# Performance work log

Hardware: AMD Instinct MI355X
Metric: run time of the kernel (lower is better)

## Reference

```python
import jax, jax.numpy as jnp
import numpy as np

N = 100000          # nodes
E = 300000          # edges
F_IN = 128          # num_features
H = 256             # hidden_size
C = 1               # num_classes
G = 2048            # number of graphs in batch
EPS = 1e-5


def setup_inputs() -> dict:
    key = jax.random.key(0)
    ks = jax.random.split(key, 16)
    x = jax.random.normal(ks[0], (N, F_IN), dtype=jnp.float32)
    edge_index = jax.random.randint(ks[1], (2, E), 0, N, dtype=jnp.int64)
    batch = jnp.sort(jax.random.randint(ks[2], (N,), 0, G, dtype=jnp.int64))

    def glorot(k, shape):
        lim = np.sqrt(6.0 / (shape[0] + shape[1]))
        return jax.random.uniform(k, shape, jnp.float32, -lim, lim)

    return {
        "x": x, "edge_index": edge_index, "batch": batch,
        "W1": glorot(ks[3], (F_IN, H)), "b1": jnp.zeros((H,), jnp.float32),
        "W2": glorot(ks[4], (H, H)),    "b2": jnp.zeros((H,), jnp.float32),
        "W3": glorot(ks[5], (H, H)),    "b3": jnp.zeros((H,), jnp.float32),
        "g1": jnp.ones((H,), jnp.float32),  "be1": jnp.zeros((H,), jnp.float32),
        "g2": jnp.ones((H,), jnp.float32),  "be2": jnp.zeros((H,), jnp.float32),
        "g3": jnp.ones((H,), jnp.float32),  "be3": jnp.zeros((H,), jnp.float32),
        "LW1": glorot(ks[6], (H, H)),   "Lb1": jnp.zeros((H,), jnp.float32),
        "LW2": glorot(ks[7], (H, C)),   "Lb2": jnp.zeros((C,), jnp.float32),
    }


def _gcn_conv(x, W, b, src, dst, dinv):
    xw = x @ W                                       # [N, H]
    coeff = (dinv[src] * dinv[dst])[:, None]          # [E, 1]
    msg = xw[src] * coeff                             # gather + scale, [E, H]
    agg = jax.ops.segment_sum(msg, dst, num_segments=x.shape[0])  # scatter-add
    agg = agg + xw * (dinv * dinv)[:, None]           # self-loop term
    return agg + b


def _bn_relu(h, g, be):
    # BatchNorm1d in training mode: batch stats over nodes (biased variance)
    m = h.mean(axis=0)
    v = h.var(axis=0)
    return jax.nn.relu((h - m) * jax.lax.rsqrt(v + EPS) * g + be)


def reference(x, edge_index, batch, W1, b1, W2, b2, W3, b3,
              g1, be1, g2, be2, g3, be3, LW1, Lb1, LW2, Lb2):
    src = edge_index[0]
    dst = edge_index[1]
    # degree with self-loops (computed at destination, as in PyG)
    deg = jax.ops.segment_sum(jnp.ones((E,), jnp.float32), dst, num_segments=N) + 1.0
    dinv = jax.lax.rsqrt(deg)

    h = _bn_relu(_gcn_conv(x, W1, b1, src, dst, dinv), g1, be1)
    h = _bn_relu(_gcn_conv(h, W2, b2, src, dst, dinv), g2, be2)
    h = _bn_relu(_gcn_conv(h, W3, b3, src, dst, dinv), g3, be3)

    # global_add_pool: sum node features per graph
    pooled = jax.ops.segment_sum(h, batch, num_segments=G)   # [G, H]

    out = jax.nn.relu(pooled @ LW1 + Lb1)
    out = out @ LW2 + Lb2                                    # [G, 1]
    return jnp.squeeze(out, axis=1)                          # [G]
```

## Files before the change

### kernel.cpp

```cpp
#include <hip/hip_runtime.h>


typedef __attribute__((ext_vector_type(8))) short bf16x8;
typedef __attribute__((ext_vector_type(4))) float f32x4;

__device__ inline float bf2f(unsigned short u) {
    union { unsigned int i; float f; } v; v.i = ((unsigned int)u) << 16; return v.f;
}
__device__ inline unsigned short f2bf(float f) {
    unsigned int x = __float_as_uint(f);
    unsigned int r = (x + 0x7FFFu + ((x >> 16) & 1u)) >> 16;
    return (unsigned short)r;
}

__device__ inline float4 ld4u(const unsigned short* p) {
    ushort4 u = *(const ushort4*)(p);
    return make_float4(bf2f(u.x), bf2f(u.y), bf2f(u.z), bf2f(u.w));
}
__device__ inline void st4u(unsigned short* p, float4 v) {
    ushort4 u; u.x = f2bf(v.x); u.y = f2bf(v.y); u.z = f2bf(v.z); u.w = f2bf(v.w);
    *(ushort4*)p = u;
}

__global__ void count_deg_i(const int* __restrict__ dst, int* __restrict__ deg, int E) {
    int i = blockIdx.x * blockDim.x + threadIdx.x;
    int stride = gridDim.x * blockDim.x;
    for (; i < E; i += stride) atomicAdd(&deg[dst[i]], 1);
}

__global__ __launch_bounds__(256) void scan_partial(
    const int* __restrict__ deg, int* __restrict__ psum, int N)
{
    __shared__ int red[256];
    const int t = threadIdx.x;
    const int i0 = blockIdx.x * 512 + t * 2;
    int s = 0;
    if (i0 < N) s += deg[i0];
    if (i0 + 1 < N) s += deg[i0 + 1];
    red[t] = s;
    __syncthreads();
    for (int off = 128; off > 0; off >>= 1) {
        if (t < off) red[t] += red[t + off];
        __syncthreads();
    }
    if (t == 0) psum[blockIdx.x] = red[0];
}

__global__ __launch_bounds__(1024) void scan_offsets(
    const int* __restrict__ psum, int* __restrict__ poff, int NB,
    int* __restrict__ rowptr, int N)
{
    __shared__ int s[1024];
    const int t = threadIdx.x;
    int v = (t < NB) ? psum[t] : 0;
    s[t] = v;
    __syncthreads();
    for (int off = 1; off < 1024; off <<= 1) {
        int u = (t >= off) ? s[t - off] : 0;
        __syncthreads();
        s[t] += u;
        __syncthreads();
    }
    if (t < NB) poff[t] = s[t] - v;
    if (t == 1023) rowptr[N] = s[1023];
}

__global__ __launch_bounds__(256) void write_rowptr(
    const int* __restrict__ deg, const int* __restrict__ poff,
    int* __restrict__ rowptr, int N)
{
    __shared__ int s[256];
    const int t = threadIdx.x;
    const int i0 = blockIdx.x * 512 + t * 2;
    int e0 = (i0 < N) ? deg[i0] : 0;
    int e1 = (i0 + 1 < N) ? deg[i0 + 1] : 0;
    int sum = e0 + e1;
    s[t] = sum;
    __syncthreads();
    for (int off = 1; off < 256; off <<= 1) {
        int u = (t >= off) ? s[t - off] : 0;
        __syncthreads();
        s[t] += u;
        __syncthreads();
    }
    int excl = s[t] - sum + poff[blockIdx.x];
    if (i0 < N) rowptr[i0] = excl;
    if (i0 + 1 < N) rowptr[i0 + 1] = excl + e0;
}

__global__ void dinv_from_rowptr(const int* __restrict__ rowptr, float* __restrict__ dinv, int N) {
    int i = blockIdx.x * blockDim.x + threadIdx.x;
    if (i < N) dinv[i] = rsqrtf((float)(rowptr[i + 1] - rowptr[i]) + 1.0f);
}

__global__ void fill_csr(const int* __restrict__ src, const int* __restrict__ dst,
                         const int* __restrict__ rowptr, int* __restrict__ cnt,
                         int* __restrict__ col, int E)
{
    int i = blockIdx.x * blockDim.x + threadIdx.x;
    int stride = gridDim.x * blockDim.x;
    for (; i < E; i += stride) {
        int d = dst[i];
        int pos = atomicAdd(&cnt[d], 1);
        col[rowptr[d] + pos] = src[i];
    }
}

__global__ void conv_bf16(const float* __restrict__ in, unsigned short* __restrict__ out,
                          size_t n4)
{
    size_t i = blockIdx.x * (size_t)blockDim.x + threadIdx.x;
    size_t stride = (size_t)gridDim.x * blockDim.x;
    const float4* in4 = (const float4*)in;
    for (; i < n4; i += stride) {
        float4 v = in4[i];
        st4u(out + i * 4, v);
    }
}

__global__ void make_wt(const float* __restrict__ W, unsigned short* __restrict__ WT, int K) {
    int i = blockIdx.x * blockDim.x + threadIdx.x;
    if (i < K * 256) {
        int k = i >> 8, n = i & 255;
        WT[n * K + k] = f2bf(W[i]);
    }
}

__device__ inline unsigned int bn2(unsigned int w, float sL, float hL, float sH, float hH) {
    float lo = bf2f((unsigned short)(w & 0xFFFFu));
    float hi = bf2f((unsigned short)(w >> 16));
    lo = fmaxf(fmaf(lo, sL, hL), 0.f);
    hi = fmaxf(fmaf(hi, sH, hH), 0.f);
    return (unsigned int)f2bf(lo) | ((unsigned int)f2bf(hi) << 16);
}
__device__ inline uint4 bn8(uint4 v, const float* __restrict__ ss, int c) {
    float4 sA = *(const float4*)(ss + c);
    float4 sB = *(const float4*)(ss + c + 4);
    float4 hA = *(const float4*)(ss + 256 + c);
    float4 hB = *(const float4*)(ss + 256 + c + 4);
    uint4 r;
    r.x = bn2(v.x, sA.x, hA.x, sA.y, hA.y);
    r.y = bn2(v.y, sA.z, hA.z, sA.w, hA.w);
    r.z = bn2(v.z, sB.x, hB.x, sB.y, hB.y);
    r.w = bn2(v.w, sB.z, hB.z, sB.w, hB.w);
    return r;
}

template<int FUSE_BN>
__global__ __launch_bounds__(256) void gemm_mfma(
    const unsigned short* __restrict__ A,
    const unsigned short* __restrict__ WT,
    const float* __restrict__ dinv,
    const float* __restrict__ ss,
    unsigned short* __restrict__ C,
    int K)
{
    __shared__ unsigned short As[128 * 32];
    __shared__ unsigned short Bs[128 * 32];

    const int tid = threadIdx.x;
    const int bm = blockIdx.x * 128;
    const int bn = blockIdx.y * 128;
    const int lane = tid & 63;
    const int wid = tid >> 6;
    const int wr = wid >> 1;
    const int wc = wid & 1;

    const int r0 = tid >> 2;
    const int cc0 = tid & 3;

    f32x4 acc[4][4];
    #pragma unroll
    for (int m = 0; m < 4; ++m)
        #pragma unroll
        for (int n = 0; n < 4; ++n)
            acc[m][n] = (f32x4){0.f, 0.f, 0.f, 0.f};

    uint4* AsV = (uint4*)As;
    uint4* BsV = (uint4*)Bs;

    for (int k0 = 0; k0 < K; k0 += 32) {
        if (k0) __syncthreads();
        {
            const int gcc = (cc0 ^ (r0 & 3)) * 8;
            uint4 va0 = *(const uint4*)(A  + (size_t)(bm + r0)      * K + k0 + gcc);
            uint4 vb0 = *(const uint4*)(WT + (size_t)(bn + r0)      * K + k0 + gcc);
            uint4 va1 = *(const uint4*)(A  + (size_t)(bm + r0 + 64) * K + k0 + gcc);
            uint4 vb1 = *(const uint4*)(WT + (size_t)(bn + r0 + 64) * K + k0 + gcc);
            if (FUSE_BN) {
                va0 = bn8(va0, ss, k0 + gcc);
                va1 = bn8(va1, ss, k0 + gcc);
            }
            AsV[r0 * 4 + cc0]        = va0;
            AsV[(r0 + 64) * 4 + cc0] = va1;
            BsV[r0 * 4 + cc0]        = vb0;
            BsV[(r0 + 64) * 4 + cc0] = vb1;
        }
        __syncthreads();

        bf16x8 af[4], bfv[4];
        #pragma unroll
        for (int n = 0; n < 4; ++n) {
            int R = wc * 64 + n * 16 + (lane & 15);
            int pc = (lane >> 4) ^ (R & 3);
            af[n] = *(const bf16x8*)&Bs[R * 32 + pc * 8];
        }
        #pragma unroll
        for (int m = 0; m < 4; ++m) {
            int R = wr * 64 + m * 16 + (lane & 15);
            int pc = (lane >> 4) ^ (R & 3);
            bfv[m] = *(const bf16x8*)&As[R * 32 + pc * 8];
        }
        #pragma unroll
        for (int m = 0; m < 4; ++m)
            #pragma unroll
            for (int n = 0; n < 4; ++n)
                acc[m][n] = __builtin_amdgcn_mfma_f32_16x16x32_bf16(
                    af[n], bfv[m], acc[m][n], 0, 0, 0);
    }

    #pragma unroll
    for (int m = 0; m < 4; ++m) {
        int row = bm + wr * 64 + m * 16 + (lane & 15);
        float di = dinv[row];
        #pragma unroll
        for (int n = 0; n < 4; ++n) {
            int cb = bn + wc * 64 + n * 16 + ((lane >> 4) << 2);
            ushort4 u;
            u.x = f2bf(acc[m][n][0] * di);
            u.y = f2bf(acc[m][n][1] * di);
            u.z = f2bf(acc[m][n][2] * di);
            u.w = f2bf(acc[m][n][3] * di);
            *(ushort4*)(C + (size_t)row * 256 + cb) = u;
        }
    }
}

__global__ __launch_bounds__(256) void gather_bn(
    const unsigned short* __restrict__ xs, const int* __restrict__ rowptr,
    const int* __restrict__ col, const float* __restrict__ dinv,
    const float* __restrict__ b, unsigned short* __restrict__ t_out,
    float* __restrict__ stats, int N)
{
    __shared__ float lred[4][512];
    const int lane = threadIdx.x & 63;
    const int wid = threadIdx.x >> 6;
    const int c4 = lane * 4;
    const float4 bv = *(const float4*)(b + c4);

    float s0 = 0, s1 = 0, s2 = 0, s3 = 0;
    float q0 = 0, q1 = 0, q2 = 0, q3 = 0;

    const int w = (blockIdx.x * blockDim.x + threadIdx.x) >> 6;
    const int nw = (gridDim.x * blockDim.x) >> 6;

    for (int n0 = w; n0 < N; n0 += nw * 4) {
        const int nA = n0;
        const int nB = n0 + nw;
        const int nC = n0 + 2 * nw;
        const int nD = n0 + 3 * nw;
        const bool hB = nB < N, hC = nC < N, hD = nD < N;

        int eA = rowptr[nA], eA1 = rowptr[nA + 1];
        int eB = 0, eB1 = 0, eC = 0, eC1 = 0, eD = 0, eD1 = 0;
        if (hB) { eB = rowptr[nB]; eB1 = rowptr[nB + 1]; }
        if (hC) { eC = rowptr[nC]; eC1 = rowptr[nC + 1]; }
        if (hD) { eD = rowptr[nD]; eD1 = rowptr[nD + 1]; }

        float4 aA = ld4u(xs + (size_t)nA * 256 + c4);
        float4 aB = make_float4(0.f, 0.f, 0.f, 0.f), aC = aB, aD = aB;
        if (hB) aB = ld4u(xs + (size_t)nB * 256 + c4);
        if (hC) aC = ld4u(xs + (size_t)nC * 256 + c4);
        if (hD) aD = ld4u(xs + (size_t)nD * 256 + c4);

        while ((eA < eA1) | (eB < eB1) | (eC < eC1) | (eD < eD1)) {
            int sA = -1, sB = -1, sC = -1, sD = -1;
            if (eA < eA1) sA = col[eA++];
            if (eB < eB1) sB = col[eB++];
            if (eC < eC1) sC = col[eC++];
            if (eD < eD1) sD = col[eD++];
            float4 vA, vB, vC, vD;
            if (sA >= 0) vA = ld4u(xs + (size_t)sA * 256 + c4);
            if (sB >= 0) vB = ld4u(xs + (size_t)sB * 256 + c4);
            if (sC >= 0) vC = ld4u(xs + (size_t)sC * 256 + c4);
            if (sD >= 0) vD = ld4u(xs + (size_t)sD * 256 + c4);
            if (sA >= 0) { aA.x += vA.x; aA.y += vA.y; aA.z += vA.z; aA.w += vA.w; }
            if (sB >= 0) { aB.x += vB.x; aB.y += vB.y; aB.z += vB.z; aB.w += vB.w; }
            if (sC >= 0) { aC.x += vC.x; aC.y += vC.y; aC.z += vC.z; aC.w += vC.w; }
            if (sD >= 0) { aD.x += vD.x; aD.y += vD.y; aD.z += vD.z; aD.w += vD.w; }
        }

        {
            float di = dinv[nA];
            float4 t;
            t.x = fmaf(di, aA.x, bv.x); t.y = fmaf(di, aA.y, bv.y);
            t.z = fmaf(di, aA.z, bv.z); t.w = fmaf(di, aA.w, bv.w);
            st4u(t_out + (size_t)nA * 256 + c4, t);
            s0 += t.x; s1 += t.y; s2 += t.z; s3 += t.w;
            q0 += t.x * t.x; q1 += t.y * t.y; q2 += t.z * t.z; q3 += t.w * t.w;
        }
        if (hB) {
            float di = dinv[nB];
            float4 t;
            t.x = fmaf(di, aB.x, bv.x); t.y = fmaf(di, aB.y, bv.y);
            t.z = fmaf(di, aB.z, bv.z); t.w = fmaf(di, aB.w, bv.w);
            st4u(t_out + (size_t)nB * 256 + c4, t);
            s0 += t.x; s1 += t.y; s2 += t.z; s3 += t.w;
            q0 += t.x * t.x; q1 += t.y * t.y; q2 += t.z * t.z; q3 += t.w * t.w;
        }
        if (hC) {
            float di = dinv[nC];
            float4 t;
            t.x = fmaf(di, aC.x, bv.x); t.y = fmaf(di, aC.y, bv.y);
            t.z = fmaf(di, aC.z, bv.z); t.w = fmaf(di, aC.w, bv.w);
            st4u(t_out + (size_t)nC * 256 + c4, t);
            s0 += t.x; s1 += t.y; s2 += t.z; s3 += t.w;
            q0 += t.x * t.x; q1 += t.y * t.y; q2 += t.z * t.z; q3 += t.w * t.w;
        }
        if (hD) {
            float di = dinv[nD];
            float4 t;
            t.x = fmaf(di, aD.x, bv.x); t.y = fmaf(di, aD.y, bv.y);
            t.z = fmaf(di, aD.z, bv.z); t.w = fmaf(di, aD.w, bv.w);
            st4u(t_out + (size_t)nD * 256 + c4, t);
            s0 += t.x; s1 += t.y; s2 += t.z; s3 += t.w;
            q0 += t.x * t.x; q1 += t.y * t.y; q2 += t.z * t.z; q3 += t.w * t.w;
        }
    }

    lred[wid][c4 + 0] = s0; lred[wid][c4 + 1] = s1;
    lred[wid][c4 + 2] = s2; lred[wid][c4 + 3] = s3;
    lred[wid][256 + c4 + 0] = q0; lred[wid][256 + c4 + 1] = q1;
    lred[wid][256 + c4 + 2] = q2; lred[wid][256 + c4 + 3] = q3;
    __syncthreads();
    for (int i = threadIdx.x; i < 512; i += 256) {
        float v = lred[0][i] + lred[1][i] + lred[2][i] + lred[3][i];
        atomicAdd(&stats[i], v);
    }
}

__global__ void bn_finalize(const float* __restrict__ stats,
                            const float* __restrict__ g, const float* __restrict__ be,
                            float* __restrict__ ss, int N)
{
    int f = threadIdx.x;
    float m = stats[f] / (float)N;
    float v = stats[256 + f] / (float)N - m * m;
    float sc = g[f] * rsqrtf(v + 1e-5f);
    ss[f] = sc;
    ss[256 + f] = be[f] - m * sc;
}

__global__ __launch_bounds__(256) void pool_seg(
    const unsigned short* __restrict__ t, const int* __restrict__ batch,
    const float* __restrict__ ss, float* __restrict__ pooled, int N)
{
    __shared__ float lred[4][256];
    const int g = blockIdx.x;
    const int lane = threadIdx.x & 63;
    const int wid = threadIdx.x >> 6;
    const int c4 = lane * 4;

    int lo = 0, hi = N;
    while (lo < hi) { int m = (lo + hi) >> 1; if (batch[m] < g) lo = m + 1; else hi = m; }
    const int start = lo;
    hi = N;
    while (lo < hi) { int m = (lo + hi) >> 1; if (batch[m] < g + 1) lo = m + 1; else hi = m; }
    const int end = lo;

    const float4 sc = *(const float4*)(ss + c4);
    const float4 sh = *(const float4*)(ss + 256 + c4);
    float4 acc = make_float4(0.f, 0.f, 0.f, 0.f);
    for (int r = start + wid; r < end; r += 4) {
        float4 a = ld4u(t + (size_t)r * 256 + c4);
        acc.x += fmaxf(fmaf(a.x, sc.x, sh.x), 0.f);
        acc.y += fmaxf(fmaf(a.y, sc.y, sh.y), 0.f);
        acc.z += fmaxf(fmaf(a.z, sc.z, sh.z), 0.f);
        acc.w += fmaxf(fmaf(a.w, sc.w, sh.w), 0.f);
    }
    lred[wid][c4 + 0] = acc.x; lred[wid][c4 + 1] = acc.y;
    lred[wid][c4 + 2] = acc.z; lred[wid][c4 + 3] = acc.w;
    __syncthreads();
    int i = threadIdx.x;
    pooled[(size_t)g * 256 + i] = lred[0][i] + lred[1][i] + lred[2][i] + lred[3][i];
}

__global__ __launch_bounds__(256) void mlp_fused(
    const float* __restrict__ pooled,
    const float* __restrict__ LW1, const float* __restrict__ Lb1,
    const float* __restrict__ LW2, const float* __restrict__ Lb2,
    float* __restrict__ out)
{
    __shared__ float sp[256];
    __shared__ float red[256];
    const int g = blockIdx.x;
    const int t = threadIdx.x;
    sp[t] = pooled[(size_t)g * 256 + t];
    __syncthreads();
    float acc = Lb1[t];
    #pragma unroll 8
    for (int k = 0; k < 256; ++k) acc = fmaf(sp[k], LW1[k * 256 + t], acc);
    acc = fmaxf(acc, 0.f);
    red[t] = acc * LW2[t];
    __syncthreads();
    for (int s = 128; s > 0; s >>= 1) {
        if (t < s) red[t] += red[t + s];
        __syncthreads();
    }
    if (t == 0) out[g] = red[0] + Lb2[0];
}

extern "C" void kernel_launch(void* const* d_in, const int* in_sizes, int n_in,
                              void* d_out, int out_size, void* d_ws, size_t ws_size,
                              hipStream_t stream)
{
    const float* x    = (const float*)d_in[0];
    const int*   ei   = (const int*)d_in[1];
    const int*   batch= (const int*)d_in[2];
    const float* W1 = (const float*)d_in[3];  const float* b1 = (const float*)d_in[4];
    const float* W2 = (const float*)d_in[5];  const float* b2 = (const float*)d_in[6];
    const float* W3 = (const float*)d_in[7];  const float* b3 = (const float*)d_in[8];
    const float* g1 = (const float*)d_in[9];  const float* be1= (const float*)d_in[10];
    const float* g2 = (const float*)d_in[11]; const float* be2= (const float*)d_in[12];
    const float* g3 = (const float*)d_in[13]; const float* be3= (const float*)d_in[14];
    const float* LW1= (const float*)d_in[15]; const float* Lb1= (const float*)d_in[16];
    const float* LW2= (const float*)d_in[17]; const float* Lb2= (const float*)d_in[18];

    const int N = in_sizes[2];
    const int E = in_sizes[1] / 2;
    const int F = in_sizes[0] / N;
    const int H = in_sizes[4];
    const int G = out_size;
    const int Mp = (N + 127) & ~127;
    const int NB = (N + 511) / 512;
    const int* src = ei;
    const int* dst = ei + E;
    const size_t NHp = (size_t)Mp * H;

    const float* Wl[3] = {W1, W2, W3};
    const float* bl[3] = {b1, b2, b3};
    const float* gl[3] = {g1, g2, g3};
    const float* bel[3]= {be1, be2, be3};

    char* p = (char*)d_ws;
    unsigned short* TB = (unsigned short*)p;  p += NHp * 2;
    unsigned short* XS = (unsigned short*)p;  p += NHp * 2;
    unsigned short* XB = (unsigned short*)p;  p += (size_t)Mp * 128 * 2;
    float* dinv = (float*)p;           p += (((size_t)Mp * 4) + 255) & ~(size_t)255;
    int* degi  = (int*)p;              p += (((size_t)N * 4) + 255) & ~(size_t)255;
    float* stats = (float*)p;          p += 2048;
    float* ss    = (float*)p;          p += 2048;
    int* psum   = (int*)p;             p += 4096;
    int* poff   = (int*)p;             p += 4096;
    float* pooled= (float*)p;          p += (size_t)G * H * 4;
    int* rowptr = (int*)p;             p += (((size_t)(N + 1) * 4) + 255) & ~(size_t)255;
    int* col    = (int*)p;             p += (((size_t)E * 4) + 255) & ~(size_t)255;
    unsigned short* WTb = (unsigned short*)p;  p += (size_t)H * H * 2;

    hipMemsetAsync(degi, 0, (size_t)N * sizeof(int), stream);
    count_deg_i<<<1024, 256, 0, stream>>>(dst, degi, E);
    scan_partial<<<NB, 256, 0, stream>>>(degi, psum, N);
    scan_offsets<<<1, 1024, 0, stream>>>(psum, poff, NB, rowptr, N);
    write_rowptr<<<NB, 256, 0, stream>>>(degi, poff, rowptr, N);
    dinv_from_rowptr<<<(N + 255) / 256, 256, 0, stream>>>(rowptr, dinv, N);
    hipMemsetAsync(degi, 0, (size_t)N * sizeof(int), stream);
    fill_csr<<<1024, 256, 0, stream>>>(src, dst, rowptr, degi, col, E);

    conv_bf16<<<2048, 256, 0, stream>>>(x, XB, (size_t)N * F / 4);

    for (int L = 0; L < 3; ++L) {
        const int K = (L == 0) ? F : H;
        make_wt<<<(K * 256 + 255) / 256, 256, 0, stream>>>(Wl[L], WTb, K);
        dim3 grid(Mp / 128, H / 128);
        if (L == 0)
            gemm_mfma<0><<<grid, 256, 0, stream>>>(XB, WTb, dinv, nullptr, XS, K);
        else
            gemm_mfma<1><<<grid, 256, 0, stream>>>(TB, WTb, dinv, ss, XS, K);
        hipMemsetAsync(stats, 0, 512 * sizeof(float), stream);
        gather_bn<<<1024, 256, 0, stream>>>(XS, rowptr, col, dinv, bl[L], TB, stats, N);
        bn_finalize<<<1, 256, 0, stream>>>(stats, gl[L], bel[L], ss, N);
    }

    pool_seg<<<G, 256, 0, stream>>>(TB, batch, ss, pooled, N);
    mlp_fused<<<G, 256, 0, stream>>>(pooled, LW1, Lb1, LW2, Lb2, (float*)d_out);
}
```

Baseline: 594.0 us.

## Aggregate before transform in layer one, fuse pool+MLP, batch weight prep

Layer one now aggregates the 128-wide input features over the graph before the GEMM (A·X·W ordering), so the sparse gather moves 128 columns instead of 256. Because of that it needs a separate stats pass over the GEMM output. All three weight transposes are combined into one launch. Pooling and the MLP head are fused into one kernel handling 8 graphs per block. Stats zeroing moves into bn_finalize, the GEMM gets a grouped block-index remap, and the gather grid size doubles. This changes rounding order and adds an extra full read of the layer-one output for the stats.

```diff
diff --git a/kernel.cpp b/kernel.cpp
--- a/kernel.cpp
+++ b/kernel.cpp
@@ -12,7 +12,6 @@
     unsigned int r = (x + 0x7FFFu + ((x >> 16) & 1u)) >> 16;
     return (unsigned short)r;
 }
-
 __device__ inline float4 ld4u(const unsigned short* p) {
     ushort4 u = *(const ushort4*)(p);
     return make_float4(bf2f(u.x), bf2f(u.y), bf2f(u.z), bf2f(u.w));
@@ -20,6 +19,14 @@
 __device__ inline void st4u(unsigned short* p, float4 v) {
     ushort4 u; u.x = f2bf(v.x); u.y = f2bf(v.y); u.z = f2bf(v.z); u.w = f2bf(v.w);
     *(ushort4*)p = u;
+}
+__device__ inline float2 ld2u(const unsigned short* p) {
+    ushort2 u = *(const ushort2*)(p);
+    return make_float2(bf2f(u.x), bf2f(u.y));
+}
+__device__ inline void st2u(unsigned short* p, float2 v) {
+    ushort2 u; u.x = f2bf(v.x); u.y = f2bf(v.y);
+    *(ushort2*)p = u;
 }
 
 __global__ void count_deg_i(const int* __restrict__ dst, int* __restrict__ deg, int E) {
@@ -106,23 +113,88 @@
     }
 }
 
-__global__ void conv_bf16(const float* __restrict__ in, unsigned short* __restrict__ out,
-                          size_t n4)
-{
-    size_t i = blockIdx.x * (size_t)blockDim.x + threadIdx.x;
+__global__ void make_wt_all(const float* __restrict__ W1, const float* __restrict__ W2,
+                            const float* __restrict__ W3,
+                            unsigned short* __restrict__ T1, unsigned short* __restrict__ T2,
+                            unsigned short* __restrict__ T3)
+{
+    int i = blockIdx.x * blockDim.x + threadIdx.x;
+    if (i < 128 * 256) {
+        int k = i >> 8, n = i & 255;
+        T1[n * 128 + k] = f2bf(W1[i]);
+    } else if (i < 128 * 256 + 256 * 256) {
+        int j = i - 128 * 256;
+        int k = j >> 8, n = j & 255;
+        T2[n * 256 + k] = f2bf(W2[j]);
+    } else if (i < 128 * 256 + 2 * 256 * 256) {
+        int j = i - 128 * 256 - 256 * 256;
+        int k = j >> 8, n = j & 255;
+        T3[n * 256 + k] = f2bf(W3[j]);
+    }
+}
+
+__global__ void conv_xt(const float* __restrict__ in, const float* __restrict__ dinv,
+                        unsigned short* __restrict__ out, int N)
+{
+    size_t n4 = (size_t)N * 32;
     size_t stride = (size_t)gridDim.x * blockDim.x;
     const float4* in4 = (const float4*)in;
-    for (; i < n4; i += stride) {
+    for (size_t i = blockIdx.x * (size_t)blockDim.x + threadIdx.x; i < n4; i += stride) {
+        int row = (int)(i >> 5);
+        float di = dinv[row];
         float4 v = in4[i];
+        v.x *= di; v.y *= di; v.z *= di; v.w *= di;
         st4u(out + i * 4, v);
     }
 }
 
-__global__ void make_wt(const float* __restrict__ W, unsigned short* __restrict__ WT, int K) {
-    int i = blockIdx.x * blockDim.x + threadIdx.x;
-    if (i < K * 256) {
-        int k = i >> 8, n = i & 255;
-        WT[n * K + k] = f2bf(W[i]);
+__global__ __launch_bounds__(256) void gather_in(
+    const unsigned short* __restrict__ xt, const int* __restrict__ rowptr,
+    const int* __restrict__ col, const float* __restrict__ dinv,
+    unsigned short* __restrict__ aout, int N)
+{
+    const int lane = threadIdx.x & 63;
+    const int c2 = lane * 2;
+    const int w = (blockIdx.x * blockDim.x + threadIdx.x) >> 6;
+    const int nw = (gridDim.x * blockDim.x) >> 6;
+
+    for (int n0 = w; n0 < N; n0 += nw * 4) {
+        const int nA = n0, nB = n0 + nw, nC = n0 + 2 * nw, nD = n0 + 3 * nw;
+        const bool hB = nB < N, hC = nC < N, hD = nD < N;
+
+        int eA = rowptr[nA], eA1 = rowptr[nA + 1];
+        int eB = 0, eB1 = 0, eC = 0, eC1 = 0, eD = 0, eD1 = 0;
+        if (hB) { eB = rowptr[nB]; eB1 = rowptr[nB + 1]; }
+        if (hC) { eC = rowptr[nC]; eC1 = rowptr[nC + 1]; }
+        if (hD) { eD = rowptr[nD]; eD1 = rowptr[nD + 1]; }
+
+        float2 aA = ld2u(xt + (size_t)nA * 128 + c2);
+        float2 aB = make_float2(0.f, 0.f), aC = aB, aD = aB;
+        if (hB) aB = ld2u(xt + (size_t)nB * 128 + c2);
+        if (hC) aC = ld2u(xt + (size_t)nC * 128 + c2);
+        if (hD) aD = ld2u(xt + (size_t)nD * 128 + c2);
+
+        while ((eA < eA1) | (eB < eB1) | (eC < eC1) | (eD < eD1)) {
+            int sA = -1, sB = -1, sC = -1, sD = -1;
+            if (eA < eA1) sA = col[eA++];
+            if (eB < eB1) sB = col[eB++];
+            if (eC < eC1) sC = col[eC++];
+            if (eD < eD1) sD = col[eD++];
+            float2 vA, vB, vC, vD;
+            if (sA >= 0) vA = ld2u(xt + (size_t)sA * 128 + c2);
+            if (sB >= 0) vB = ld2u(xt + (size_t)sB * 128 + c2);
+            if (sC >= 0) vC = ld2u(xt + (size_t)sC * 128 + c2);
+            if (sD >= 0) vD = ld2u(xt + (size_t)sD * 128 + c2);
+            if (sA >= 0) { aA.x += vA.x; aA.y += vA.y; }
+            if (sB >= 0) { aB.x += vB.x; aB.y += vB.y; }
+            if (sC >= 0) { aC.x += vC.x; aC.y += vC.y; }
+            if (sD >= 0) { aD.x += vD.x; aD.y += vD.y; }
+        }
+
+        { float di = dinv[nA]; st2u(aout + (size_t)nA * 128 + c2, make_float2(di * aA.x, di * aA.y)); }
+        if (hB) { float di = dinv[nB]; st2u(aout + (size_t)nB * 128 + c2, make_float2(di * aB.x, di * aB.y)); }
+        if (hC) { float di = dinv[nC]; st2u(aout + (size_t)nC * 128 + c2, make_float2(di * aC.x, di * aC.y)); }
+        if (hD) { float di = dinv[nD]; st2u(aout + (size_t)nD * 128 + c2, make_float2(di * aD.x, di * aD.y)); }
     }
 }
 
@@ -146,26 +218,38 @@
     return r;
 }
 
-template<int FUSE_BN>
+template<int FUSE_BN, int EPI>
 __global__ __launch_bounds__(256) void gemm_mfma(
     const unsigned short* __restrict__ A,
     const unsigned short* __restrict__ WT,
     const float* __restrict__ dinv,
     const float* __restrict__ ss,
+    const float* __restrict__ bias,
     unsigned short* __restrict__ C,
-    int K)
-{
+    int K, int nbx)
+{
+    const int id = blockIdx.x;
+    const int main2 = (nbx & ~7) * 2;
+    int bx, by;
+    if (id < main2) {
+        bx = (id >> 4) * 8 + (id & 7);
+        by = (id >> 3) & 1;
+    } else {
+        int r = id - main2;
+        bx = (nbx & ~7) + (r >> 1);
+        by = r & 1;
+    }
+
     __shared__ unsigned short As[128 * 32];
     __shared__ unsigned short Bs[128 * 32];
 
     const int tid = threadIdx.x;
-    const int bm = blockIdx.x * 128;
-    const int bn = blockIdx.y * 128;
+    const int bm = bx * 128;
+    const int bn = by * 128;
     const int lane = tid & 63;
     const int wid = tid >> 6;
     const int wr = wid >> 1;
     const int wc = wid & 1;
-
     const int r0 = tid >> 2;
     const int cc0 = tid & 3;
 
@@ -222,18 +306,39 @@
     #pragma unroll
     for (int m = 0; m < 4; ++m) {
         int row = bm + wr * 64 + m * 16 + (lane & 15);
-        float di = dinv[row];
+        float di = (EPI == 0) ? dinv[row] : 0.f;
         #pragma unroll
         for (int n = 0; n < 4; ++n) {
             int cb = bn + wc * 64 + n * 16 + ((lane >> 4) << 2);
             ushort4 u;
-            u.x = f2bf(acc[m][n][0] * di);
-            u.y = f2bf(acc[m][n][1] * di);
-            u.z = f2bf(acc[m][n][2] * di);
-            u.w = f2bf(acc[m][n][3] * di);
+            if (EPI == 0) {
+                u.x = f2bf(acc[m][n][0] * di);
+                u.y = f2bf(acc[m][n][1] * di);
+                u.z = f2bf(acc[m][n][2] * di);
+                u.w = f2bf(acc[m][n][3] * di);
+            } else {
+                float4 bv = *(const float4*)(bias + cb);
+                u.x = f2bf(acc[m][n][0] + bv.x);
+                u.y = f2bf(acc[m][n][1] + bv.y);
+                u.z = f2bf(acc[m][n][2] + bv.z);
+                u.w = f2bf(acc[m][n][3] + bv.w);
+            }
             *(ushort4*)(C + (size_t)row * 256 + cb) = u;
         }
     }
+}
+
+__global__ __launch_bounds__(256) void t_stats(
+    const unsigned short* __restrict__ t, float* __restrict__ stats, int N)
+{
+    const int f = threadIdx.x;
+    float sum = 0.f, sq = 0.f;
+    for (int r = blockIdx.x; r < N; r += gridDim.x) {
+        float v = bf2f(t[(size_t)r * 256 + f]);
+        sum += v; sq += v * v;
+    }
+    atomicAdd(&stats[f], sum);
+    atomicAdd(&stats[256 + f], sq);
 }
 
 __global__ __launch_bounds__(256) void gather_bn(
@@ -255,10 +360,7 @@
     const int nw = (gridDim.x * blockDim.x) >> 6;
 
     for (int n0 = w; n0 < N; n0 += nw * 4) {
-        const int nA = n0;
-        const int nB = n0 + nw;
-        const int nC = n0 + 2 * nw;
-        const int nD = n0 + 3 * nw;
+        const int nA = n0, nB = n0 + nw, nC = n0 + 2 * nw, nD = n0 + 3 * nw;
         const bool hB = nB < N, hC = nC < N, hD = nD < N;
 
         int eA = rowptr[nA], eA1 = rowptr[nA + 1];
@@ -339,75 +441,86 @@
     }
 }
 
-__global__ void bn_finalize(const float* __restrict__ stats,
+__global__ void bn_finalize(float* __restrict__ stats,
                             const float* __restrict__ g, const float* __restrict__ be,
                             float* __restrict__ ss, int N)
 {
     int f = threadIdx.x;
-    float m = stats[f] / (float)N;
-    float v = stats[256 + f] / (float)N - m * m;
+    float sm = stats[f];
+    float sqv = stats[256 + f];
+    float m = sm / (float)N;
+    float v = sqv / (float)N - m * m;
     float sc = g[f] * rsqrtf(v + 1e-5f);
     ss[f] = sc;
     ss[256 + f] = be[f] - m * sc;
-}
-
-__global__ __launch_bounds__(256) void pool_seg(
+    stats[f] = 0.f;
+    stats[256 + f] = 0.f;
+}
+
+__global__ __launch_bounds__(256) void pool_mlp(
     const unsigned short* __restrict__ t, const int* __restrict__ batch,
-    const float* __restrict__ ss, float* __restrict__ pooled, int N)
-{
+    const float* __restrict__ ss,
+    const float* __restrict__ LW1, const float* __restrict__ Lb1,
+    const float* __restrict__ LW2, const float* __restrict__ Lb2,
+    float* __restrict__ out, int N, int G)
+{
+    __shared__ int bnd[9];
     __shared__ float lred[4][256];
-    const int g = blockIdx.x;
-    const int lane = threadIdx.x & 63;
-    const int wid = threadIdx.x >> 6;
+    __shared__ float sp[8][256];
+    __shared__ float wpart[4][8];
+
+    const int tid = threadIdx.x;
+    const int g0 = blockIdx.x * 8;
+    if (tid < 9) {
+        int target = g0 + tid;
+        int lo = 0, hi = N;
+        while (lo < hi) { int m = (lo + hi) >> 1; if (batch[m] < target) lo = m + 1; else hi = m; }
+        bnd[tid] = lo;
+    }
+    __syncthreads();
+
+    const int lane = tid & 63;
+    const int wid = tid >> 6;
     const int c4 = lane * 4;
-
-    int lo = 0, hi = N;
-    while (lo < hi) { int m = (lo + hi) >> 1; if (batch[m] < g) lo = m + 1; else hi = m; }
-    const int start = lo;
-    hi = N;
-    while (lo < hi) { int m = (lo + hi) >> 1; if (batch[m] < g + 1) lo = m + 1; else hi = m; }
-    const int end = lo;
-
     const float4 sc = *(const float4*)(ss + c4);
     const float4 sh = *(const float4*)(ss + 256 + c4);
-    float4 acc = make_float4(0.f, 0.f, 0.f, 0.f);
-    for (int r = start + wid; r < end; r += 4) {
-        float4 a = ld4u(t + (size_t)r * 256 + c4);
-        acc.x += fmaxf(fmaf(a.x, sc.x, sh.x), 0.f);
-        acc.y += fmaxf(fmaf(a.y, sc.y, sh.y), 0.f);
-        acc.z += fmaxf(fmaf(a.z, sc.z, sh.z), 0.f);
-        acc.w += fmaxf(fmaf(a.w, sc.w, sh.w), 0.f);
-    }
-    lred[wid][c4 + 0] = acc.x; lred[wid][c4 + 1] = acc.y;
-    lred[wid][c4 + 2] = acc.z; lred[wid][c4 + 3] = acc.w;
+
+    for (int j = 0; j < 8; ++j) {
+        float4 acc = make_float4(0.f, 0.f, 0.f, 0.f);
+        for (int r = bnd[j] + wid; r < bnd[j + 1]; r += 4) {
+            float4 a = ld4u(t + (size_t)r * 256 + c4);
+            acc.x += fmaxf(fmaf(a.x, sc.x, sh.x), 0.f);
+            acc.y += fmaxf(fmaf(a.y, sc.y, sh.y), 0.f);
+            acc.z += fmaxf(fmaf(a.z, sc.z, sh.z), 0.f);
+            acc.w += fmaxf(fmaf(a.w, sc.w, sh.w), 0.f);
+        }
+        lred[wid][c4 + 0] = acc.x; lred[wid][c4 + 1] = acc.y;
+        lred[wid][c4 + 2] = acc.z; lred[wid][c4 + 3] = acc.w;
+        __syncthreads();
+        sp[j][tid] = lred[0][tid] + lred[1][tid] + lred[2][tid] + lred[3][tid];
+        __syncthreads();
+    }
+
+    float acc8[8];
+    float b1v = Lb1[tid];
+    #pragma unroll
+    for (int j = 0; j < 8; ++j) acc8[j] = b1v;
+    for (int k = 0; k < 256; ++k) {
+        float w = LW1[k * 256 + tid];
+        #pragma unroll
+        for (int j = 0; j < 8; ++j) acc8[j] = fmaf(sp[j][k], w, acc8[j]);
+    }
+    float w2 = LW2[tid];
+    #pragma unroll
+    for (int j = 0; j < 8; ++j) {
+        float v = fmaxf(acc8[j], 0.f) * w2;
+        #pragma unroll
+        for (int off = 32; off > 0; off >>= 1) v += __shfl_down(v, off);
+        if (lane == 0) wpart[wid][j] = v;
+    }
     __syncthreads();
-    int i = threadIdx.x;
-    pooled[(size_t)g * 256 + i] = lred[0][i] + lred[1][i] + lred[2][i] + lred[3][i];
-}
-
-__global__ __launch_bounds__(256) void mlp_fused(
-    const float* __restrict__ pooled,
-    const float* __restrict__ LW1, const float* __restrict__ Lb1,
-    const float* __restrict__ LW2, const float* __restrict__ Lb2,
-    float* __restrict__ out)
-{
-    __shared__ float sp[256];
-    __shared__ float red[256];
-    const int g = blockIdx.x;
-    const int t = threadIdx.x;
-    sp[t] = pooled[(size_t)g * 256 + t];
-    __syncthreads();
-    float acc = Lb1[t];
-    #pragma unroll 8
-    for (int k = 0; k < 256; ++k) acc = fmaf(sp[k], LW1[k * 256 + t], acc);
-    acc = fmaxf(acc, 0.f);
-    red[t] = acc * LW2[t];
-    __syncthreads();
-    for (int s = 128; s > 0; s >>= 1) {
-        if (t < s) red[t] += red[t + s];
-        __syncthreads();
-    }
-    if (t == 0) out[g] = red[0] + Lb2[0];
+    if (tid < 8 && g0 + tid < G)
+        out[g0 + tid] = wpart[0][tid] + wpart[1][tid] + wpart[2][tid] + wpart[3][tid] + Lb2[0];
 }
 
 extern "C" void kernel_launch(void* const* d_in, const int* in_sizes, int n_in,
@@ -428,36 +541,32 @@
 
     const int N = in_sizes[2];
     const int E = in_sizes[1] / 2;
-    const int F = in_sizes[0] / N;
     const int H = in_sizes[4];
     const int G = out_size;
     const int Mp = (N + 127) & ~127;
     const int NB = (N + 511) / 512;
+    const int nbx = Mp / 128;
     const int* src = ei;
     const int* dst = ei + E;
     const size_t NHp = (size_t)Mp * H;
 
-    const float* Wl[3] = {W1, W2, W3};
-    const float* bl[3] = {b1, b2, b3};
-    const float* gl[3] = {g1, g2, g3};
-    const float* bel[3]= {be1, be2, be3};
-
     char* p = (char*)d_ws;
     unsigned short* TB = (unsigned short*)p;  p += NHp * 2;
     unsigned short* XS = (unsigned short*)p;  p += NHp * 2;
-    unsigned short* XB = (unsigned short*)p;  p += (size_t)Mp * 128 * 2;
     float* dinv = (float*)p;           p += (((size_t)Mp * 4) + 255) & ~(size_t)255;
     int* degi  = (int*)p;              p += (((size_t)N * 4) + 255) & ~(size_t)255;
     float* stats = (float*)p;          p += 2048;
     float* ss    = (float*)p;          p += 2048;
     int* psum   = (int*)p;             p += 4096;
     int* poff   = (int*)p;             p += 4096;
-    float* pooled= (float*)p;          p += (size_t)G * H * 4;
     int* rowptr = (int*)p;             p += (((size_t)(N + 1) * 4) + 255) & ~(size_t)255;
     int* col    = (int*)p;             p += (((size_t)E * 4) + 255) & ~(size_t)255;
-    unsigned short* WTb = (unsigned short*)p;  p += (size_t)H * H * 2;
+    unsigned short* WT1 = (unsigned short*)p;  p += (size_t)128 * 256 * 2;
+    unsigned short* WT2 = (unsigned short*)p;  p += (size_t)256 * 256 * 2;
+    unsigned short* WT3 = (unsigned short*)p;  p += (size_t)256 * 256 * 2;
 
     hipMemsetAsync(degi, 0, (size_t)N * sizeof(int), stream);
+    hipMemsetAsync(stats, 0, 512 * sizeof(float), stream);
     count_deg_i<<<1024, 256, 0, stream>>>(dst, degi, E);
     scan_partial<<<NB, 256, 0, stream>>>(degi, psum, N);
     scan_offsets<<<1, 1024, 0, stream>>>(psum, poff, NB, rowptr, N);
@@ -466,21 +575,23 @@
     hipMemsetAsync(degi, 0, (size_t)N * sizeof(int), stream);
     fill_csr<<<1024, 256, 0, stream>>>(src, dst, rowptr, degi, col, E);
 
-    conv_bf16<<<2048, 256, 0, stream>>>(x, XB, (size_t)N * F / 4);
-
-    for (int L = 0; L < 3; ++L) {
-        const int K = (L == 0) ? F : H;
-        make_wt<<<(K * 256 + 255) / 256, 256, 0, stream>>>(Wl[L], WTb, K);
-        dim3 grid(Mp / 128, H / 128);
-        if (L == 0)
-            gemm_mfma<0><<<grid, 256, 0, stream>>>(XB, WTb, dinv, nullptr, XS, K);
-        else
-            gemm_mfma<1><<<grid, 256, 0, stream>>>(TB, WTb, dinv, ss, XS, K);
-        hipMemsetAsync(stats, 0, 512 * sizeof(float), stream);
-        gather_bn<<<1024, 256, 0, stream>>>(XS, rowptr, col, dinv, bl[L], TB, stats, N);
-        bn_finalize<<<1, 256, 0, stream>>>(stats, gl[L], bel[L], ss, N);
-    }
-
-    pool_seg<<<G, 256, 0, stream>>>(TB, batch, ss, pooled, N);
-    mlp_fused<<<G, 256, 0, stream>>>(pooled, LW1, Lb1, LW2, Lb2, (float*)d_out);
-}
+    make_wt_all<<<(128 * 256 + 2 * 256 * 256 + 255) / 256, 256, 0, stream>>>(
+        W1, W2, W3, WT1, WT2, WT3);
+
+    conv_xt<<<2048, 256, 0, stream>>>(x, dinv, TB, N);
+    gather_in<<<2048, 256, 0, stream>>>(TB, rowptr, col, dinv, XS, N);
+    gemm_mfma<0, 1><<<nbx * 2, 256, 0, stream>>>(XS, WT1, dinv, nullptr, b1, TB, 128, nbx);
+    t_stats<<<1024, 256, 0, stream>>>(TB, stats, N);
+    bn_finalize<<<1, 256, 0, stream>>>(stats, g1, be1, ss, N);
+
+    gemm_mfma<1, 0><<<nbx * 2, 256, 0, stream>>>(TB, WT2, dinv, ss, nullptr, XS, 256, nbx);
+    gather_bn<<<2048, 256, 0, stream>>>(XS, rowptr, col, dinv, b2, TB, stats, N);
+    bn_finalize<<<1, 256, 0, stream>>>(stats, g2, be2, ss, N);
+
+    gemm_mfma<1, 0><<<nbx * 2, 256, 0, stream>>>(TB, WT3, dinv, ss, nullptr, XS, 256, nbx);
+    gather_bn<<<2048, 256, 0, stream>>>(XS, rowptr, col, dinv, b3, TB, stats, N);
+    bn_finalize<<<1, 256, 0, stream>>>(stats, g3, be3, ss, N);
+
+    pool_mlp<<<(G + 7) / 8, 256, 0, stream>>>(TB, batch, ss, LW1, Lb1, LW2, Lb2,
+                                              (float*)d_out, N, G);
+}
```

Measured after the change: 626.3 us. +5.4%, slower.
